# Kernel optimization log

Measured on AMD Instinct MI355X. Metric: run time of the kernel, lower is better.

## Reference

```python
import jax, jax.numpy as jnp
import numpy as np

DELTA_VAR = 0.5
DELTA_DIST = 1.5
ALPHA, BETA, GAMMA = 1.0, 1.0, 0.001
NUM_CLUSTERS = 16  # labels in [0, 16); all assumed present per sample (N >> C)

B, F, N = 32, 8, 131072


def _l1(x, axis):
    return jnp.sum(jnp.abs(x), axis=axis)  # norm=1 in the original module


def _discriminative_loss(x, target):
    # x: (B, F, N) float, target: (B, N) int labels in [0, C)
    b, f, n = x.shape
    c = NUM_CLUSTERS
    # flatten batch+cluster into one segment id space
    seg = (target + jnp.arange(b, dtype=target.dtype)[:, None] * c).reshape(-1)  # (B*N,)
    x_flat = x.transpose(0, 2, 1).reshape(b * n, f)  # (B*N, F)

    sums = jax.ops.segment_sum(x_flat, seg, num_segments=b * c)              # (B*C, F)
    counts = jax.ops.segment_sum(jnp.ones((b * n,), x.dtype), seg, num_segments=b * c)
    present = counts > 0
    safe_cnt = jnp.where(present, counts, 1.0)
    means_c = sums / safe_cnt[:, None]                                        # (B*C, F) per-cluster means

    # per-point cluster mean (== c_means tensor in torch, shape (B,F,N) there)
    means_pt = means_c[seg]                                                   # (B*N, F)

    # variance term: hinge(||x - mean||_1 - delta_var)^2, averaged per cluster, summed
    var = jnp.maximum(_l1(x_flat - means_pt, axis=1) - DELTA_VAR, 0.0) ** 2   # (B*N,)
    var_sums = jax.ops.segment_sum(var, seg, num_segments=b * c)
    # NOTE: torch version's division by num_clusters is a discarded no-op -> only /bs
    var_term = jnp.sum(jnp.where(present, var_sums / safe_cnt, 0.0)) / b

    # distance term: torch indexes c_means[i][:, unique_labels]; with labels 0..C-1
    # present, unique == arange(C), i.e. the per-point means at point indices 0..C-1
    mc = means_pt.reshape(b, n, f)[:, :c, :]                                  # (B, C, F)
    d = _l1(mc[:, :, None, :] - mc[:, None, :, :], axis=-1)                   # (B, C, C)
    margin = 2.0 * DELTA_DIST * (1.0 - jnp.eye(c, dtype=x.dtype))             # (C, C)
    dist = jnp.sum(jnp.maximum(margin[None] - d, 0.0) ** 2, axis=(1, 2)) / (c * (c - 1))
    dist_term = jnp.sum(dist) / b

    # regularization: mean over (distinct) cluster means of their L1 norm
    mcC = means_c.reshape(b, c, f)
    reg_term = jnp.sum(jnp.mean(_l1(mcC, axis=-1), axis=1)) / b

    return ALPHA * var_term + BETA * dist_term + GAMMA * reg_term


def setup_inputs() -> dict:
    key = jax.random.key(0)
    kx, kt = jax.random.split(key)
    x = jax.random.normal(kx, (B, F, N), dtype=jnp.float32)
    target = jax.random.randint(kt, (B, N), 0, NUM_CLUSTERS, dtype=jnp.int64)
    return {"input": x, "target": target}


def reference(input, target):
    return _discriminative_loss(input, target)
```

## Files before the change

kernel.cpp:

```cpp
#include <hip/hip_runtime.h>

#define BB 32
#define FF 8
#define NN 131072
#define CC 16

#define CHUNKS 64
#define POINTS (NN / CHUNKS)
#define NBLK   (CHUNKS * BB)

constexpr float DELTA_VAR  = 0.5f;
constexpr float DELTA_DIST = 1.5f;
constexpr float ALPHA = 1.0f, BETA = 1.0f, GAMMA = 0.001f;

#define PSLOT    160
#define WS_PART  0
#define NPART    (NBLK * PSLOT)
#define WS_VARB  NPART
#define WS_DRG   (NPART + 32)
#define WS_CNTI  (NPART + 64)

__global__ __launch_bounds__(256) void k_sums(const float* __restrict__ x,
                                              const int* __restrict__ tgt,
                                              float* __restrict__ ws,
                                              int* __restrict__ wsi) {
    __shared__ float priv[256 * 34];
    __shared__ float cpriv[64 * 17];
    const int tid = threadIdx.x;
    const int b  = blockIdx.y;
    const int ch = blockIdx.x;

    if (ch == 0 && tid == 0) { ws[WS_VARB + b] = 0.f; ws[WS_DRG + b] = 0.f; }
    if (ch == 0 && b == 0 && tid == 1) wsi[WS_CNTI] = 0;

#pragma unroll
    for (int i = 0; i < 34; ++i) priv[tid * 34 + i] = 0.f;
    if (tid < 64) {
#pragma unroll
        for (int i = 0; i < 16; ++i) cpriv[tid * 17 + i] = 0.f;
    }
    __syncthreads();

    const int fp = tid >> 6;
    const int g  = tid & 63;
    const int n0 = ch * POINTS;
    const float* __restrict__ xf0 = x + (size_t)b * FF * NN + (size_t)(2 * fp) * NN;
    const float* __restrict__ xf1 = xf0 + NN;
    const int*   __restrict__ tb  = tgt + (size_t)b * NN;
    const int base  = tid * 34;
    const int cbase = g * 17;

#pragma unroll 2
    for (int k = 0; k < POINTS / 128; ++k) {
        const int n = n0 + k * 128 + g * 2;
        const int2   t2 = *reinterpret_cast<const int2*>(tb + n);
        const float2 v0 = *reinterpret_cast<const float2*>(xf0 + n);
        const float2 v1 = *reinterpret_cast<const float2*>(xf1 + n);
        {
            float2* p = reinterpret_cast<float2*>(&priv[base + 2 * t2.x]);
            float2 cur = *p; cur.x += v0.x; cur.y += v1.x; *p = cur;
        }
        {
            float2* p = reinterpret_cast<float2*>(&priv[base + 2 * t2.y]);
            float2 cur = *p; cur.x += v0.y; cur.y += v1.y; *p = cur;
        }
        if (fp == 0) {
            cpriv[cbase + t2.x] += 1.f;
            cpriv[cbase + t2.y] += 1.f;
        }
    }
    __syncthreads();

    float* const part = &ws[WS_PART + (size_t)(b * CHUNKS + ch) * PSLOT];
    if (tid < 128) {
        const int f = tid >> 4, c = tid & 15;
        const int pair = f >> 1, comp = f & 1;
        float s = 0.f;
#pragma unroll
        for (int gg = 0; gg < 64; ++gg)
            s += priv[(pair * 64 + gg) * 34 + 2 * c + comp];
        part[tid] = s;
    } else if (tid < 144) {
        const int rc = tid - 128;
        float s = 0.f;
#pragma unroll
        for (int gg = 0; gg < 64; ++gg) s += cpriv[gg * 17 + rc];
        part[tid] = s;
    }
}

__global__ __launch_bounds__(256) void k_var(const float* __restrict__ x,
                                             const int* __restrict__ tgt,
                                             float* __restrict__ ws,
                                             int* __restrict__ wsi,
                                             float* __restrict__ out) {
    __shared__ float sred[144];
    __shared__ float smf[CC * 12];
    __shared__ float sinv[CC];
    __shared__ float wsum[4];
    __shared__ float sdist[CC];
    __shared__ int   sst[CC];
    __shared__ int   lastflag;

    const int tid = threadIdx.x;
    const int b   = blockIdx.y;
    const int ch  = blockIdx.x;

    if (tid < 144) {
        const float* p = &ws[WS_PART + (size_t)b * CHUNKS * PSLOT + tid];
        float s = 0.f;
#pragma unroll 8
        for (int c2 = 0; c2 < CHUNKS; ++c2) s += p[(size_t)c2 * PSLOT];
        sred[tid] = s;
    }
    if (ch == 0 && tid >= 144 && tid < 160) sst[tid - 144] = tgt[(size_t)b * NN + (tid - 144)];
    __syncthreads();
    if (tid < CC) {
        const float cnt = sred[128 + tid];
        sinv[tid] = cnt > 0.f ? 1.f / cnt : 0.f;
    }
    __syncthreads();
    if (tid < 128) {
        const int f = tid >> 4, c = tid & 15;
        smf[c * 12 + f] = sred[tid] * sinv[c];
    }
    __syncthreads();

    if (ch == 0 && tid < CC) {
        const int c = tid;
        float l1 = 0.f;
#pragma unroll
        for (int f = 0; f < FF; ++f) l1 += fabsf(smf[c * 12 + f]);
        const int ti = sst[c];
        float mi[FF];
#pragma unroll
        for (int f = 0; f < FF; ++f) mi[f] = smf[ti * 12 + f];
        float dsum = 0.f;
        for (int j = 0; j < CC; ++j) {
            const int tj = sst[j];
            float d = 0.f;
#pragma unroll
            for (int f = 0; f < FF; ++f) d += fabsf(mi[f] - smf[tj * 12 + f]);
            if (j != c) {
                const float h = 2.f * DELTA_DIST - d;
                if (h > 0.f) dsum += h * h;
            }
        }
        sdist[c] = (GAMMA / (float)(CC * BB)) * l1
                 + (BETA / (float)(CC * (CC - 1) * BB)) * dsum;
    }

    const float4* sm4 = reinterpret_cast<const float4*>(smf);
    const int n0 = ch * POINTS;
    const float* __restrict__ xb = x + (size_t)b * FF * NN;
    const int*   __restrict__ tb = tgt + (size_t)b * NN;

    float acc = 0.f;
#pragma unroll
    for (int it = 0; it < 2; ++it) {
        const int n = n0 + tid * 4 + it * 1024;
        const int4 t4 = *reinterpret_cast<const int4*>(tb + n);
        const float4 A0 = sm4[3 * t4.x], B0 = sm4[3 * t4.x + 1];
        const float4 A1 = sm4[3 * t4.y], B1 = sm4[3 * t4.y + 1];
        const float4 A2 = sm4[3 * t4.z], B2 = sm4[3 * t4.z + 1];
        const float4 A3 = sm4[3 * t4.w], B3 = sm4[3 * t4.w + 1];
        float s0, s1, s2, s3;
        {
            const float4 v = *reinterpret_cast<const float4*>(xb + 0 * NN + n);
            s0 = fabsf(v.x - A0.x); s1 = fabsf(v.y - A1.x);
            s2 = fabsf(v.z - A2.x); s3 = fabsf(v.w - A3.x);
        }
        {
            const float4 v = *reinterpret_cast<const float4*>(xb + 1 * NN + n);
            s0 += fabsf(v.x - A0.y); s1 += fabsf(v.y - A1.y);
            s2 += fabsf(v.z - A2.y); s3 += fabsf(v.w - A3.y);
        }
        {
            const float4 v = *reinterpret_cast<const float4*>(xb + 2 * NN + n);
            s0 += fabsf(v.x - A0.z); s1 += fabsf(v.y - A1.z);
            s2 += fabsf(v.z - A2.z); s3 += fabsf(v.w - A3.z);
        }
        {
            const float4 v = *reinterpret_cast<const float4*>(xb + 3 * NN + n);
            s0 += fabsf(v.x - A0.w); s1 += fabsf(v.y - A1.w);
            s2 += fabsf(v.z - A2.w); s3 += fabsf(v.w - A3.w);
        }
        {
            const float4 v = *reinterpret_cast<const float4*>(xb + 4 * NN + n);
            s0 += fabsf(v.x - B0.x); s1 += fabsf(v.y - B1.x);
            s2 += fabsf(v.z - B2.x); s3 += fabsf(v.w - B3.x);
        }
        {
            const float4 v = *reinterpret_cast<const float4*>(xb + 5 * NN + n);
            s0 += fabsf(v.x - B0.y); s1 += fabsf(v.y - B1.y);
            s2 += fabsf(v.z - B2.y); s3 += fabsf(v.w - B3.y);
        }
        {
            const float4 v = *reinterpret_cast<const float4*>(xb + 6 * NN + n);
            s0 += fabsf(v.x - B0.z); s1 += fabsf(v.y - B1.z);
            s2 += fabsf(v.z - B2.z); s3 += fabsf(v.w - B3.z);
        }
        {
            const float4 v = *reinterpret_cast<const float4*>(xb + 7 * NN + n);
            s0 += fabsf(v.x - B0.w); s1 += fabsf(v.y - B1.w);
            s2 += fabsf(v.z - B2.w); s3 += fabsf(v.w - B3.w);
        }
        float h;
        h = fmaxf(s0 - DELTA_VAR, 0.f); acc += h * h * sinv[t4.x];
        h = fmaxf(s1 - DELTA_VAR, 0.f); acc += h * h * sinv[t4.y];
        h = fmaxf(s2 - DELTA_VAR, 0.f); acc += h * h * sinv[t4.z];
        h = fmaxf(s3 - DELTA_VAR, 0.f); acc += h * h * sinv[t4.w];
    }

#pragma unroll
    for (int off = 32; off > 0; off >>= 1) acc += __shfl_down(acc, off, 64);
    if ((tid & 63) == 0) wsum[tid >> 6] = acc;
    __syncthreads();

    if (tid == 0) {
        atomicAdd(&ws[WS_VARB + b], wsum[0] + wsum[1] + wsum[2] + wsum[3]);
        if (ch == 0) {
            float drg = 0.f;
#pragma unroll
            for (int i = 0; i < CC; ++i) drg += sdist[i];
            atomicAdd(&ws[WS_DRG + b], drg);
        }
        asm volatile("s_waitcnt vmcnt(0)" ::: "memory");
        lastflag = (atomicAdd(&wsi[WS_CNTI], 1) == NBLK - 1);
    }
    __syncthreads();
    if (lastflag && tid < 64) {
        float val = 0.f;
        if (tid < BB) {
            const float v = atomicAdd(&ws[WS_VARB + tid], 0.f);
            const float d = atomicAdd(&ws[WS_DRG + tid], 0.f);
            val = (ALPHA / (float)BB) * v + d;
        }
#pragma unroll
        for (int off = 16; off > 0; off >>= 1) val += __shfl_down(val, off, 64);
        if (tid == 0) out[0] = val;
    }
}

extern "C" void kernel_launch(void* const* d_in, const int* in_sizes, int n_in,
                              void* d_out, int out_size, void* d_ws, size_t ws_size,
                              hipStream_t stream) {
    const float* x  = (const float*)d_in[0];
    const int* tgt  = (const int*)d_in[1];
    float* out = (float*)d_out;
    float* ws  = (float*)d_ws;
    int*   wsi = (int*)d_ws;

    dim3 grid(CHUNKS, BB);
    k_sums<<<grid, 256, 0, stream>>>(x, tgt, ws, wsi);
    k_var <<<grid, 256, 0, stream>>>(x, tgt, ws, wsi, out);
}
```

Baseline: 68.94 us.

## Use one feature per thread group with float4 loads and restructure final reduction

The sums kernel now assigns one feature per 32-thread group and loads float4 of x and int4 of labels, which halves the shared-memory private histograms and changes the LDS update pattern. The distance/regularization computation in the variance kernel moves after the main loop, reading labels directly and reducing with shuffles instead of shared arrays. The last-block detection via atomic counter return value is replaced by a designated block spinning until all blocks have arrived, which removes a barrier in other blocks but relies on that block not starving others (deadlock risk if not all blocks are resident).

```diff
diff --git a/kernel.cpp b/kernel.cpp
--- a/kernel.cpp
+++ b/kernel.cpp
@@ -24,8 +24,8 @@
                                               const int* __restrict__ tgt,
                                               float* __restrict__ ws,
                                               int* __restrict__ wsi) {
-    __shared__ float priv[256 * 34];
-    __shared__ float cpriv[64 * 17];
+    __shared__ float priv[256 * 17];
+    __shared__ float cpriv[32 * 17];
     const int tid = threadIdx.x;
     const int b  = blockIdx.y;
     const int ch = blockIdx.x;
@@ -34,57 +34,51 @@
     if (ch == 0 && b == 0 && tid == 1) wsi[WS_CNTI] = 0;
 
 #pragma unroll
-    for (int i = 0; i < 34; ++i) priv[tid * 34 + i] = 0.f;
-    if (tid < 64) {
+    for (int i = 0; i < 16; ++i) priv[tid * 17 + i] = 0.f;
+    if (tid < 32) {
 #pragma unroll
         for (int i = 0; i < 16; ++i) cpriv[tid * 17 + i] = 0.f;
     }
     __syncthreads();
 
-    const int fp = tid >> 6;
-    const int g  = tid & 63;
+    const int f  = tid >> 5;
+    const int g  = tid & 31;
     const int n0 = ch * POINTS;
-    const float* __restrict__ xf0 = x + (size_t)b * FF * NN + (size_t)(2 * fp) * NN;
-    const float* __restrict__ xf1 = xf0 + NN;
-    const int*   __restrict__ tb  = tgt + (size_t)b * NN;
-    const int base  = tid * 34;
+    const float* __restrict__ xf = x + (size_t)b * FF * NN + (size_t)f * NN;
+    const int*   __restrict__ tb = tgt + (size_t)b * NN;
+    const int base  = tid * 17;
     const int cbase = g * 17;
 
 #pragma unroll 2
     for (int k = 0; k < POINTS / 128; ++k) {
-        const int n = n0 + k * 128 + g * 2;
-        const int2   t2 = *reinterpret_cast<const int2*>(tb + n);
-        const float2 v0 = *reinterpret_cast<const float2*>(xf0 + n);
-        const float2 v1 = *reinterpret_cast<const float2*>(xf1 + n);
-        {
-            float2* p = reinterpret_cast<float2*>(&priv[base + 2 * t2.x]);
-            float2 cur = *p; cur.x += v0.x; cur.y += v1.x; *p = cur;
-        }
-        {
-            float2* p = reinterpret_cast<float2*>(&priv[base + 2 * t2.y]);
-            float2 cur = *p; cur.x += v0.y; cur.y += v1.y; *p = cur;
-        }
-        if (fp == 0) {
-            cpriv[cbase + t2.x] += 1.f;
-            cpriv[cbase + t2.y] += 1.f;
+        const int n = n0 + k * 128 + g * 4;
+        const int4   t4 = *reinterpret_cast<const int4*>(tb + n);
+        const float4 v  = *reinterpret_cast<const float4*>(xf + n);
+        priv[base + t4.x] += v.x;
+        priv[base + t4.y] += v.y;
+        priv[base + t4.z] += v.z;
+        priv[base + t4.w] += v.w;
+        if (f == 0) {
+            cpriv[cbase + t4.x] += 1.f;
+            cpriv[cbase + t4.y] += 1.f;
+            cpriv[cbase + t4.z] += 1.f;
+            cpriv[cbase + t4.w] += 1.f;
         }
     }
     __syncthreads();
 
     float* const part = &ws[WS_PART + (size_t)(b * CHUNKS + ch) * PSLOT];
     if (tid < 128) {
-        const int f = tid >> 4, c = tid & 15;
-        const int pair = f >> 1, comp = f & 1;
+        const int rf = tid >> 4, rc = tid & 15;
         float s = 0.f;
 #pragma unroll
-        for (int gg = 0; gg < 64; ++gg)
-            s += priv[(pair * 64 + gg) * 34 + 2 * c + comp];
+        for (int gg = 0; gg < 32; ++gg) s += priv[(rf * 32 + gg) * 17 + rc];
         part[tid] = s;
     } else if (tid < 144) {
         const int rc = tid - 128;
         float s = 0.f;
 #pragma unroll
-        for (int gg = 0; gg < 64; ++gg) s += cpriv[gg * 17 + rc];
+        for (int gg = 0; gg < 32; ++gg) s += cpriv[gg * 17 + rc];
         part[tid] = s;
     }
 }
@@ -98,9 +92,6 @@
     __shared__ float smf[CC * 12];
     __shared__ float sinv[CC];
     __shared__ float wsum[4];
-    __shared__ float sdist[CC];
-    __shared__ int   sst[CC];
-    __shared__ int   lastflag;
 
     const int tid = threadIdx.x;
     const int b   = blockIdx.y;
@@ -113,7 +104,6 @@
         for (int c2 = 0; c2 < CHUNKS; ++c2) s += p[(size_t)c2 * PSLOT];
         sred[tid] = s;
     }
-    if (ch == 0 && tid >= 144 && tid < 160) sst[tid - 144] = tgt[(size_t)b * NN + (tid - 144)];
     __syncthreads();
     if (tid < CC) {
         const float cnt = sred[128 + tid];
@@ -125,30 +115,6 @@
         smf[c * 12 + f] = sred[tid] * sinv[c];
     }
     __syncthreads();
-
-    if (ch == 0 && tid < CC) {
-        const int c = tid;
-        float l1 = 0.f;
-#pragma unroll
-        for (int f = 0; f < FF; ++f) l1 += fabsf(smf[c * 12 + f]);
-        const int ti = sst[c];
-        float mi[FF];
-#pragma unroll
-        for (int f = 0; f < FF; ++f) mi[f] = smf[ti * 12 + f];
-        float dsum = 0.f;
-        for (int j = 0; j < CC; ++j) {
-            const int tj = sst[j];
-            float d = 0.f;
-#pragma unroll
-            for (int f = 0; f < FF; ++f) d += fabsf(mi[f] - smf[tj * 12 + f]);
-            if (j != c) {
-                const float h = 2.f * DELTA_DIST - d;
-                if (h > 0.f) dsum += h * h;
-            }
-        }
-        sdist[c] = (GAMMA / (float)(CC * BB)) * l1
-                 + (BETA / (float)(CC * (CC - 1) * BB)) * dsum;
-    }
 
     const float4* sm4 = reinterpret_cast<const float4*>(smf);
     const int n0 = ch * POINTS;
@@ -217,19 +183,51 @@
     if ((tid & 63) == 0) wsum[tid >> 6] = acc;
     __syncthreads();
 
+    float contrib = 0.f;
+    if (ch == 0 && tid < CC) {
+        const int c = tid;
+        int labs[CC];
+#pragma unroll
+        for (int j = 0; j < CC; ++j) labs[j] = tb[j];
+        float l1 = 0.f;
+#pragma unroll
+        for (int f = 0; f < FF; ++f) l1 += fabsf(smf[c * 12 + f]);
+        const int ti = labs[c];
+        float mi[FF];
+#pragma unroll
+        for (int f = 0; f < FF; ++f) mi[f] = smf[ti * 12 + f];
+        float dsum = 0.f;
+        for (int j = 0; j < CC; ++j) {
+            const int tj = labs[j];
+            float d = 0.f;
+#pragma unroll
+            for (int f = 0; f < FF; ++f) d += fabsf(mi[f] - smf[tj * 12 + f]);
+            if (j != c) {
+                const float h = 2.f * DELTA_DIST - d;
+                if (h > 0.f) dsum += h * h;
+            }
+        }
+        contrib = (GAMMA / (float)(CC * BB)) * l1
+                + (BETA / (float)(CC * (CC - 1) * BB)) * dsum;
+    }
+    if (ch == 0) {
+#pragma unroll
+        for (int off = 8; off > 0; off >>= 1) contrib += __shfl_down(contrib, off, 64);
+    }
+
     if (tid == 0) {
         atomicAdd(&ws[WS_VARB + b], wsum[0] + wsum[1] + wsum[2] + wsum[3]);
-        if (ch == 0) {
-            float drg = 0.f;
-#pragma unroll
-            for (int i = 0; i < CC; ++i) drg += sdist[i];
-            atomicAdd(&ws[WS_DRG + b], drg);
-        }
+        if (ch == 0) atomicAdd(&ws[WS_DRG + b], contrib);
         asm volatile("s_waitcnt vmcnt(0)" ::: "memory");
-        lastflag = (atomicAdd(&wsi[WS_CNTI], 1) == NBLK - 1);
-    }
-    __syncthreads();
-    if (lastflag && tid < 64) {
+        atomicAdd(&wsi[WS_CNTI], 1);
+    }
+
+    if (b == BB - 1 && ch == CHUNKS - 1) {
+        if (tid == 0) {
+            while (atomicAdd(&wsi[WS_CNTI], 0) < NBLK)
+                __builtin_amdgcn_s_sleep(8);
+        }
+        __syncthreads();
         float val = 0.f;
         if (tid < BB) {
             const float v = atomicAdd(&ws[WS_VARB + tid], 0.f);
```

Result: no change. 68.33 us (-0.9%).
